# Kernel optimization log

Measured on AMD Instinct MI355X. Metric: run time of the kernel, lower is better.

Reference implementation:

```python
import jax, jax.numpy as jnp
import numpy as np


def setup_inputs() -> dict:
    key = jax.random.key(0)
    ks = jax.random.split(key, 5)
    B, S, C = 512, 512, 96
    emissions = jax.random.normal(ks[0], (B, S, C), dtype=jnp.float32)
    tags = jax.random.randint(ks[1], (B, S), 0, C, dtype=jnp.int64)
    masks = jnp.ones((B, S), dtype=bool)
    start_transitions = jax.random.uniform(ks[2], (C,), jnp.float32, -0.1, 0.1)
    end_transitions = jax.random.uniform(ks[3], (C,), jnp.float32, -0.1, 0.1)
    transitions = jax.random.uniform(ks[4], (C, C), jnp.float32, -0.1, 0.1)
    return {
        "emissions": emissions,
        "tags": tags,
        "masks": masks,
        "start_transitions": start_transitions,
        "end_transitions": end_transitions,
        "transitions": transitions,
    }


def _crf_llh(emissions, tags, masks, start_transitions, end_transitions, transitions):
    # to time-major: (S, B, C), (S, B)
    emissions = jnp.swapaxes(emissions, 0, 1)
    tags = jnp.swapaxes(tags, 0, 1)
    masks = jnp.swapaxes(masks, 0, 1)
    S, B, C = emissions.shape
    maskf = masks.astype(emissions.dtype)

    # ---- numerator: score of the gold tag path (fully vectorized over time) ----
    em_scores = jnp.take_along_axis(emissions, tags[:, :, None], axis=2)[:, :, 0]  # (S, B)
    trans_scores = transitions[tags[:-1], tags[1:]]  # (S-1, B)
    score = start_transitions[tags[0]] + em_scores[0]
    score = score + jnp.sum((trans_scores + em_scores[1:]) * maskf[1:], axis=0)
    seq_ends = masks.astype(jnp.int32).sum(axis=0) - 1  # (B,)
    last_tags = tags[seq_ends, jnp.arange(B)]
    numerator = score + end_transitions[last_tags]

    # ---- denominator: forward algorithm (sequential logsumexp recurrence) ----
    alpha0 = start_transitions[None, :] + emissions[0]  # (B, C)

    def step(alpha, inp):
        em_i, m_i = inp  # (B, C), (B,)
        # (B, C_prev, C_next)
        scores = alpha[:, :, None] + transitions[None, :, :] + em_i[:, None, :]
        next_alpha = jax.scipy.special.logsumexp(scores, axis=1)
        alpha = jnp.where(m_i[:, None], next_alpha, alpha)
        return alpha, None

    alpha, _ = jax.lax.scan(step, alpha0, (emissions[1:], masks[1:]))
    denominator = jax.scipy.special.logsumexp(alpha + end_transitions[None, :], axis=1)

    return jnp.mean(numerator - denominator)


def reference(emissions, tags, masks, start_transitions, end_transitions, transitions):
    return _crf_llh(emissions, tags, masks, start_transitions, end_transitions, transitions)
```

## Files before the change

kernel.cpp:

```cpp
#include <hip/hip_runtime.h>
#include <hip/hip_bf16.h>
#include <math.h>


#define BATCH 512
#define SEQ   512
#define NC    96
#define NTHR  64
#define NEG_INF (-1e30f)
#define SC    0.25f
#define LSC   1.3862943611198906f

typedef __fp16 half2v __attribute__((ext_vector_type(2)));

#define WAVE_LDS_FENCE() asm volatile("s_waitcnt lgkmcnt(0)" ::: "memory")

#define DPP_STEP_F(v, op, ctrl)                                              \
    v = op(v, __int_as_float(__builtin_amdgcn_update_dpp(                    \
            __float_as_int(v), __float_as_int(v), (ctrl), 0xf, 0xf, false)))

__device__ __forceinline__ float wave_max_all(float v) {
    DPP_STEP_F(v, fmaxf, 0x111);
    DPP_STEP_F(v, fmaxf, 0x112);
    DPP_STEP_F(v, fmaxf, 0x114);
    DPP_STEP_F(v, fmaxf, 0x118);
    DPP_STEP_F(v, fmaxf, 0x142);
    DPP_STEP_F(v, fmaxf, 0x143);
    return __int_as_float(__builtin_amdgcn_readlane(__float_as_int(v), 63));
}
__device__ __forceinline__ float fadd_(float a, float b) { return a + b; }
__device__ __forceinline__ float wave_sum_all(float v) {
    DPP_STEP_F(v, fadd_, 0x111);
    DPP_STEP_F(v, fadd_, 0x112);
    DPP_STEP_F(v, fadd_, 0x114);
    DPP_STEP_F(v, fadd_, 0x118);
    DPP_STEP_F(v, fadd_, 0x142);
    DPP_STEP_F(v, fadd_, 0x143);
    return __int_as_float(__builtin_amdgcn_readlane(__float_as_int(v), 63));
}

__global__ __launch_bounds__(NTHR, 1)
void crf_llh_kernel(const float* __restrict__ em,
                    const int*   __restrict__ tags,
                    const int*   __restrict__ masks,
                    const float* __restrict__ startT,
                    const float* __restrict__ endT,
                    const float* __restrict__ trans,
                    float*       __restrict__ out)
{
    const int b = blockIdx.x;
    const int l = threadIdx.x;
    const bool active = (l < 48);
    const int j0 = active ? 2 * l     : 0;
    const int j1 = active ? 2 * l + 1 : 0;
    const int lr = (l < 48) ? l : (l - 48);

    __shared__ __align__(16) half2v qsh[48];

    const float* em_b    = em    + (size_t)b * SEQ * NC;
    const int*   tags_b  = tags  + b * SEQ;
    const int*   masks_b = masks + b * SEQ;

    half2v e0[48], e1[48];
    #pragma unroll
    for (int k = 0; k < 48; ++k) {
        const float t00 = trans[(2 * k)     * NC + j0];
        const float t01 = trans[(2 * k + 1) * NC + j0];
        const float t10 = trans[(2 * k)     * NC + j1];
        const float t11 = trans[(2 * k + 1) * NC + j1];
        e0[k] = __builtin_amdgcn_cvt_pkrtz(__expf(t00), __expf(t01));
        e1[k] = __builtin_amdgcn_cvt_pkrtz(__expf(t10), __expf(t11));
    }

    float a0 = active ? (startT[j0] + em_b[j0]) : NEG_INF;
    float a1 = active ? (startT[j1] + em_b[j1]) : NEG_INF;
    float m  = wave_max_all(fmaxf(a0, a1));

    const float2* em2 = reinterpret_cast<const float2*>(em_b);
    float2 emA = em2[1 * (NC / 2) + lr];
    float2 emB = em2[2 * (NC / 2) + lr];
    float2 emC = em2[3 * (NC / 2) + lr];
    int mkA = masks_b[1];
    int mkB = masks_b[2];
    int mkC = masks_b[3];

    for (int s = 1; s < SEQ; ++s) {
        const int sp = (s + 3 < SEQ) ? (s + 3) : (SEQ - 1);
        const float2 emN = em2[sp * (NC / 2) + lr];
        const int    mkN = masks_b[sp];

        const float wm = wave_max_all(fmaxf(a0, a1));

        const float p0 = __expf(a0 - m) * SC;
        const float p1 = __expf(a1 - m) * SC;
        const half2v ph = __builtin_amdgcn_cvt_pkrtz(p0, p1);
        if (active) qsh[l] = ph;
        WAVE_LDS_FENCE();

        float acc0a = 0.f, acc0b = 0.f, acc1a = 0.f, acc1b = 0.f;
        const uint4* q4 = reinterpret_cast<const uint4*>(qsh);
        #pragma unroll
        for (int t = 0; t < 12; ++t) {
            const uint4 qv = q4[t];
            const half2v qx = __builtin_bit_cast(half2v, qv.x);
            const half2v qy = __builtin_bit_cast(half2v, qv.y);
            const half2v qz = __builtin_bit_cast(half2v, qv.z);
            const half2v qw = __builtin_bit_cast(half2v, qv.w);
            acc0a = __builtin_amdgcn_fdot2(qx, e0[4 * t + 0], acc0a, false);
            acc1a = __builtin_amdgcn_fdot2(qx, e1[4 * t + 0], acc1a, false);
            acc0a = __builtin_amdgcn_fdot2(qy, e0[4 * t + 1], acc0a, false);
            acc1a = __builtin_amdgcn_fdot2(qy, e1[4 * t + 1], acc1a, false);
            acc0b = __builtin_amdgcn_fdot2(qz, e0[4 * t + 2], acc0b, false);
            acc1b = __builtin_amdgcn_fdot2(qz, e1[4 * t + 2], acc1b, false);
            acc0b = __builtin_amdgcn_fdot2(qw, e0[4 * t + 3], acc0b, false);
            acc1b = __builtin_amdgcn_fdot2(qw, e1[4 * t + 3], acc1b, false);
        }
        const float acc0 = acc0a + acc0b;
        const float acc1 = acc1a + acc1b;

        const bool upd = active && (mkA != 0);
        const float na0 = m + __logf(acc0) + LSC + emA.x;
        const float na1 = m + __logf(acc1) + LSC + emA.y;
        a0 = upd ? na0 : a0;
        a1 = upd ? na1 : a1;
        m = wm;

        emA = emB; emB = emC; emC = emN;
        mkA = mkB; mkB = mkC; mkC = mkN;
    }

    const float v0 = active ? (a0 + endT[j0]) : NEG_INF;
    const float v1 = active ? (a1 + endT[j1]) : NEG_INF;
    const float M  = wave_max_all(fmaxf(v0, v1));
    const float e  = active ? (__expf(v0 - M) + __expf(v1 - M)) : 0.f;
    const float denom = M + __logf(wave_sum_all(e));

    float nsum = 0.f;
    float msum = 0.f;
    #pragma unroll
    for (int k = 0; k < SEQ / NTHR; ++k) {
        const int s  = l + NTHR * k;
        const int tg = tags_b[s];
        const int mk = masks_b[s];
        msum += (mk ? 1.f : 0.f);
        if (s == 0) {
            nsum += startT[tg] + em_b[tg];
        } else if (mk) {
            nsum += trans[tags_b[s - 1] * NC + tg] + em_b[s * NC + tg];
        }
    }
    nsum = wave_sum_all(nsum);
    msum = wave_sum_all(msum);
    if (l == 0) {
        const int cnt  = (int)msum;
        const int last = tags_b[cnt - 1];
        atomicAdd(out, (nsum + endT[last] - denom) * (1.0f / (float)BATCH));
    }
}

extern "C" void kernel_launch(void* const* d_in, const int* in_sizes, int n_in,
                              void* d_out, int out_size, void* d_ws, size_t ws_size,
                              hipStream_t stream) {
    const float* em     = (const float*)d_in[0];
    const int*   tags   = (const int*)  d_in[1];
    const int*   masks  = (const int*)  d_in[2];
    const float* startT = (const float*)d_in[3];
    const float* endT   = (const float*)d_in[4];
    const float* trans  = (const float*)d_in[5];
    float* out = (float*)d_out;

    (void)hipMemsetAsync(out, 0, sizeof(float), stream);
    crf_llh_kernel<<<BATCH, NTHR, 0, stream>>>(em, tags, masks, startT, endT, trans, out);
}
```

Measured before the change: 428.2 us.

## Rewrite CRF forward recurrence in scaled linear domain with two-wave column split

The forward recurrence now carries alpha as scaled linear-domain weights instead of log-domain values. Each step applies a power-of-two exponent rescale taken from the previous step's max, and the exponents are accumulated into an integer sum, which removes the per-step log and the dependent max-then-exp chain. The block grows to two waves, one tag column per thread, with double-buffered LDS and an s_barrier for the cross-wave max exchange. The cost is a workgroup barrier every step and fp16 range risks in the linear weights.

```diff
diff --git a/kernel.cpp b/kernel.cpp
--- a/kernel.cpp
+++ b/kernel.cpp
@@ -6,14 +6,12 @@
 #define BATCH 512
 #define SEQ   512
 #define NC    96
-#define NTHR  64
-#define NEG_INF (-1e30f)
-#define SC    0.25f
-#define LSC   1.3862943611198906f
+#define NTHR  128
+#define LN2   0.69314718055994531f
 
 typedef __fp16 half2v __attribute__((ext_vector_type(2)));
 
-#define WAVE_LDS_FENCE() asm volatile("s_waitcnt lgkmcnt(0)" ::: "memory")
+#define BARRIER() asm volatile("s_waitcnt lgkmcnt(0)\n\ts_barrier" ::: "memory")
 
 #define DPP_STEP_F(v, op, ctrl)                                              \
     v = op(v, __int_as_float(__builtin_amdgcn_update_dpp(                    \
@@ -48,101 +46,107 @@
                     const float* __restrict__ trans,
                     float*       __restrict__ out)
 {
-    const int b = blockIdx.x;
-    const int l = threadIdx.x;
-    const bool active = (l < 48);
-    const int j0 = active ? 2 * l     : 0;
-    const int j1 = active ? 2 * l + 1 : 0;
-    const int lr = (l < 48) ? l : (l - 48);
+    const int b    = blockIdx.x;
+    const int tid  = threadIdx.x;
+    const int lane = tid & 63;
+    const int wid  = tid >> 6;
+    const bool active = (tid < NC);
+    const int jc = active ? tid : 0;
 
-    __shared__ __align__(16) half2v qsh[48];
+    __shared__ __align__(16) __fp16 qsh[2][128];
+    __shared__ float maxsh[2][2];
+    __shared__ float redn[2], redm[2], redd[2];
 
     const float* em_b    = em    + (size_t)b * SEQ * NC;
     const int*   tags_b  = tags  + b * SEQ;
     const int*   masks_b = masks + b * SEQ;
 
-    half2v e0[48], e1[48];
+    half2v ecol[48];
     #pragma unroll
     for (int k = 0; k < 48; ++k) {
-        const float t00 = trans[(2 * k)     * NC + j0];
-        const float t01 = trans[(2 * k + 1) * NC + j0];
-        const float t10 = trans[(2 * k)     * NC + j1];
-        const float t11 = trans[(2 * k + 1) * NC + j1];
-        e0[k] = __builtin_amdgcn_cvt_pkrtz(__expf(t00), __expf(t01));
-        e1[k] = __builtin_amdgcn_cvt_pkrtz(__expf(t10), __expf(t11));
+        ecol[k] = __builtin_amdgcn_cvt_pkrtz(
+            __expf(trans[(2 * k)     * NC + jc]),
+            __expf(trans[(2 * k + 1) * NC + jc]));
     }
 
-    float a0 = active ? (startT[j0] + em_b[j0]) : NEG_INF;
-    float a1 = active ? (startT[j1] + em_b[j1]) : NEG_INF;
-    float m  = wave_max_all(fmaxf(a0, a1));
+    const float al0 = startT[jc] + em_b[jc];
+    {
+        const float wm = wave_max_all(active ? al0 : -1e30f);
+        if (lane == 0) maxsh[0][wid] = wm;
+    }
+    BARRIER();
+    const float M0 = fmaxf(maxsh[0][0], maxsh[0][1]);
+    float wreg = active ? __expf(al0 - M0) : 0.f;
+    qsh[1][tid] = (__fp16)wreg;
+    BARRIER();
 
-    const float2* em2 = reinterpret_cast<const float2*>(em_b);
-    float2 emA = em2[1 * (NC / 2) + lr];
-    float2 emB = em2[2 * (NC / 2) + lr];
-    float2 emC = em2[3 * (NC / 2) + lr];
-    int mkA = masks_b[1];
-    int mkB = masks_b[2];
-    int mkC = masks_b[3];
+    int K    = 1;
+    int sumk = 0;
+
+    float emA = em_b[1 * NC + jc];
+    float emB = em_b[2 * NC + jc];
+    float emC = em_b[3 * NC + jc];
+    int mkA = masks_b[1], mkB = masks_b[2], mkC = masks_b[3];
 
     for (int s = 1; s < SEQ; ++s) {
+        const int rb = s & 1;
         const int sp = (s + 3 < SEQ) ? (s + 3) : (SEQ - 1);
-        const float2 emN = em2[sp * (NC / 2) + lr];
-        const int    mkN = masks_b[sp];
+        const float emN = em_b[sp * NC + jc];
+        const int   mkN = masks_b[sp];
 
-        const float wm = wave_max_all(fmaxf(a0, a1));
+        const uint4* q4p = reinterpret_cast<const uint4*>(&qsh[rb][0]);
+        uint4 qv[12];
+        #pragma unroll
+        for (int t = 0; t < 12; ++t) qv[t] = q4p[t];
 
-        const float p0 = __expf(a0 - m) * SC;
-        const float p1 = __expf(a1 - m) * SC;
-        const half2v ph = __builtin_amdgcn_cvt_pkrtz(p0, p1);
-        if (active) qsh[l] = ph;
-        WAVE_LDS_FENCE();
-
-        float acc0a = 0.f, acc0b = 0.f, acc1a = 0.f, acc1b = 0.f;
-        const uint4* q4 = reinterpret_cast<const uint4*>(qsh);
+        float acc[6] = {0.f, 0.f, 0.f, 0.f, 0.f, 0.f};
         #pragma unroll
         for (int t = 0; t < 12; ++t) {
-            const uint4 qv = q4[t];
-            const half2v qx = __builtin_bit_cast(half2v, qv.x);
-            const half2v qy = __builtin_bit_cast(half2v, qv.y);
-            const half2v qz = __builtin_bit_cast(half2v, qv.z);
-            const half2v qw = __builtin_bit_cast(half2v, qv.w);
-            acc0a = __builtin_amdgcn_fdot2(qx, e0[4 * t + 0], acc0a, false);
-            acc1a = __builtin_amdgcn_fdot2(qx, e1[4 * t + 0], acc1a, false);
-            acc0a = __builtin_amdgcn_fdot2(qy, e0[4 * t + 1], acc0a, false);
-            acc1a = __builtin_amdgcn_fdot2(qy, e1[4 * t + 1], acc1a, false);
-            acc0b = __builtin_amdgcn_fdot2(qz, e0[4 * t + 2], acc0b, false);
-            acc1b = __builtin_amdgcn_fdot2(qz, e1[4 * t + 2], acc1b, false);
-            acc0b = __builtin_amdgcn_fdot2(qw, e0[4 * t + 3], acc0b, false);
-            acc1b = __builtin_amdgcn_fdot2(qw, e1[4 * t + 3], acc1b, false);
+            const half2v qx = __builtin_bit_cast(half2v, qv[t].x);
+            const half2v qy = __builtin_bit_cast(half2v, qv[t].y);
+            const half2v qz = __builtin_bit_cast(half2v, qv[t].z);
+            const half2v qw = __builtin_bit_cast(half2v, qv[t].w);
+            acc[(4 * t + 0) % 6] = __builtin_amdgcn_fdot2(qx, ecol[4 * t + 0], acc[(4 * t + 0) % 6], false);
+            acc[(4 * t + 1) % 6] = __builtin_amdgcn_fdot2(qy, ecol[4 * t + 1], acc[(4 * t + 1) % 6], false);
+            acc[(4 * t + 2) % 6] = __builtin_amdgcn_fdot2(qz, ecol[4 * t + 2], acc[(4 * t + 2) % 6], false);
+            acc[(4 * t + 3) % 6] = __builtin_amdgcn_fdot2(qw, ecol[4 * t + 3], acc[(4 * t + 3) % 6], false);
         }
-        const float acc0 = acc0a + acc0b;
-        const float acc1 = acc1a + acc1b;
+        const float U = ((acc[0] + acc[1]) + (acc[2] + acc[3])) + (acc[4] + acc[5]);
 
-        const bool upd = active && (mkA != 0);
-        const float na0 = m + __logf(acc0) + LSC + emA.x;
-        const float na1 = m + __logf(acc1) + LSC + emA.y;
-        a0 = upd ? na0 : a0;
-        a1 = upd ? na1 : a1;
-        m = wm;
+        const float F = __expf(emA);
+        float w = ldexpf(U, -(K + 6)) * F;
+        if (!active) w = 0.f;
+        w = mkA ? w : wreg;
+        sumk += mkA ? (K + 6) : 0;
+        wreg = w;
+
+        const float wmx = wave_max_all(w);
+        if (lane == 0) maxsh[rb][wid] = wmx;
+        qsh[rb ^ 1][tid] = (__fp16)w;
+        BARRIER();
+
+        const float r = fmaxf(maxsh[rb][0], maxsh[rb][1]);
+        K = (int)((__float_as_uint(r) >> 23) & 255u) - 126;
 
         emA = emB; emB = emC; emC = emN;
         mkA = mkB; mkB = mkC; mkC = mkN;
     }
 
-    const float v0 = active ? (a0 + endT[j0]) : NEG_INF;
-    const float v1 = active ? (a1 + endT[j1]) : NEG_INF;
-    const float M  = wave_max_all(fmaxf(v0, v1));
-    const float e  = active ? (__expf(v0 - M) + __expf(v1 - M)) : 0.f;
-    const float denom = M + __logf(wave_sum_all(e));
+    const float dv = active ? wreg * __expf(endT[jc]) : 0.f;
+    {
+        const float ws = wave_sum_all(dv);
+        if (lane == 0) redd[wid] = ws;
+    }
+    __syncthreads();
+    const float denom = M0 + (float)sumk * LN2 + __logf(redd[0] + redd[1]);
 
-    float nsum = 0.f;
-    float msum = 0.f;
+    float nsum = 0.f, msum = 0.f;
     #pragma unroll
-    for (int k = 0; k < SEQ / NTHR; ++k) {
-        const int s  = l + NTHR * k;
+    for (int kk = 0; kk < SEQ / NTHR; ++kk) {
+        const int s  = tid + NTHR * kk;
         const int tg = tags_b[s];
         const int mk = masks_b[s];
-        msum += (mk ? 1.f : 0.f);
+        msum += mk ? 1.f : 0.f;
         if (s == 0) {
             nsum += startT[tg] + em_b[tg];
         } else if (mk) {
@@ -151,10 +155,13 @@
     }
     nsum = wave_sum_all(nsum);
     msum = wave_sum_all(msum);
-    if (l == 0) {
-        const int cnt  = (int)msum;
-        const int last = tags_b[cnt - 1];
-        atomicAdd(out, (nsum + endT[last] - denom) * (1.0f / (float)BATCH));
+    if (lane == 0) { redn[wid] = nsum; redm[wid] = msum; }
+    __syncthreads();
+    if (tid == 0) {
+        const float numer = redn[0] + redn[1];
+        const int   cnt   = (int)(redm[0] + redm[1]);
+        const int   last  = tags_b[cnt - 1];
+        atomicAdd(out, (numer + endT[last] - denom) * (1.0f / (float)BATCH));
     }
 }
 
```

New measurement: 403.4 us. 5.8% less time.
